# Performance work log

Hardware: AMD Instinct MI355X
Metric: run time of the kernel (lower is better)

## Reference

```python
import jax, jax.numpy as jnp
import numpy as np

B, S, H, E, V, P = 64, 1024, 512, 512, 32000, 40


def setup_inputs() -> dict:
    key = jax.random.key(0)
    ks = jax.random.split(key, 18)
    s = 0.05  # weight scale to keep tanh/sigmoid in active range
    inp = {}
    inp["input_token"] = jax.random.randint(ks[0], (B,), 0, V, dtype=jnp.int32)
    inp["hidden"] = jax.random.normal(ks[1], (1, B, H), jnp.float32)
    inp["cell"] = jax.random.normal(ks[2], (1, B, H), jnp.float32)
    inp["encoder_outputs"] = jax.random.normal(ks[3], (B, S, H), jnp.float32)
    pos_ids = jax.random.randint(ks[4], (B, S), 0, P)
    inp["pos_onehot"] = jax.nn.one_hot(pos_ids, P, dtype=jnp.float32)
    inp["src_mask"] = jnp.zeros((B, S), dtype=bool)  # no PAD (avoids all -inf rows)
    # learned parameters (torch Linear convention: y = x @ W.T + b)
    inp["embed_table"] = jax.random.normal(ks[5], (V, E), jnp.float32) * s
    inp["W_s"] = jax.random.normal(ks[6], (H, H), jnp.float32) * s
    inp["W_h"] = jax.random.normal(ks[7], (H, H), jnp.float32) * s
    inp["V_w"] = jax.random.normal(ks[8], (H,), jnp.float32) * s
    inp["W_p"] = jax.random.normal(ks[9], (P,), jnp.float32) * s
    inp["b_p"] = jax.random.normal(ks[10], (), jnp.float32) * s
    inp["W_ih"] = jax.random.normal(ks[11], (4 * H, E + H), jnp.float32) * s
    inp["W_hh"] = jax.random.normal(ks[12], (4 * H, H), jnp.float32) * s
    inp["b_ih"] = jax.random.normal(ks[13], (4 * H,), jnp.float32) * s
    inp["b_hh"] = jax.random.normal(ks[14], (4 * H,), jnp.float32) * s
    inp["W_out"] = jax.random.normal(ks[15], (V, H), jnp.float32) * s
    inp["b_out"] = jax.random.normal(ks[16], (V,), jnp.float32) * s
    return inp


def reference(input_token, hidden, cell, encoder_outputs, pos_onehot, src_mask,
              embed_table, W_s, W_h, V_w, W_p, b_p,
              W_ih, W_hh, b_ih, b_hh, W_out, b_out):
    # embedding (dropout is identity in eval)
    emb = embed_table[input_token]                                  # (B, E)
    q = hidden[-1]                                                  # (B, H)
    # POS-gated Bahdanau attention
    qs = q @ W_s.T                                                  # (B, H)
    eh = jnp.einsum('bsh,kh->bsk', encoder_outputs, W_h)            # (B, S, H)
    energy = jnp.tanh(qs[:, None, :] + eh)                          # (B, S, H)
    scores = jnp.einsum('bsh,h->bs', energy, V_w)                   # (B, S)
    gate = jax.nn.sigmoid(pos_onehot @ W_p + b_p)                   # (B, S)
    gated = jnp.where(src_mask, jnp.float32(-1e30), scores * gate)
    attn = jax.nn.softmax(gated, axis=-1)                           # (B, S)
    context = jnp.einsum('bs,bsh->bh', attn, encoder_outputs)       # (B, H)
    # single-step, single-layer LSTM (torch gate order: i, f, g, o)
    lstm_in = jnp.concatenate([emb, context], axis=-1)              # (B, E+H)
    gates = lstm_in @ W_ih.T + hidden[0] @ W_hh.T + b_ih + b_hh     # (B, 4H)
    i, f, g, o = jnp.split(gates, 4, axis=-1)
    c1 = jax.nn.sigmoid(f) * cell[0] + jax.nn.sigmoid(i) * jnp.tanh(g)
    h1 = jax.nn.sigmoid(o) * jnp.tanh(c1)                           # (B, H)
    pred = h1 @ W_out.T + b_out                                     # (B, V)
    return (pred, h1[None], c1[None], attn)
```

## Files before the change

kernel.cpp:

```cpp
#include <hip/hip_runtime.h>

#define BB 64
#define SS 1024
#define HH 512
#define EE 512
#define VV 32000
#define PP 40

typedef __attribute__((ext_vector_type(8))) __bf16 bf16x8;
typedef __attribute__((ext_vector_type(4))) float f32x4;
typedef __attribute__((ext_vector_type(8))) unsigned short us8_t;
typedef __attribute__((ext_vector_type(4))) unsigned short us4_t;

__device__ inline float fast_tanh(float x) {
    float e = __expf(-2.0f * fabsf(x));
    float t = (1.0f - e) / (1.0f + e);
    return copysignf(t, x);
}
__device__ inline float sigmf(float x) { return 1.0f / (1.0f + __expf(-x)); }

__device__ inline unsigned int cvtpk(float lo, float hi) {
    unsigned int r;
    asm("v_cvt_pk_bf16_f32 %0, %1, %2" : "=v"(r) : "v"(lo), "v"(hi));
    return r;
}
__device__ inline us8_t pack8c(float4 x, float4 y) {
    union { unsigned int u[4]; us8_t v; } r;
    r.u[0] = cvtpk(x.x, x.y); r.u[1] = cvtpk(x.z, x.w);
    r.u[2] = cvtpk(y.x, y.y); r.u[3] = cvtpk(y.z, y.w);
    return r.v;
}
__device__ inline us8_t pack8v(f32x4 a, f32x4 b) {
    union { unsigned int u[4]; us8_t v; } r;
    r.u[0] = cvtpk(a[0], a[1]); r.u[1] = cvtpk(a[2], a[3]);
    r.u[2] = cvtpk(b[0], b[1]); r.u[3] = cvtpk(b[2], b[3]);
    return r.v;
}

typedef __attribute__((address_space(1))) const unsigned char gas_t;
typedef __attribute__((address_space(3))) unsigned char las_t;
__device__ inline void gload16(const void* g, void* l) {
    __builtin_amdgcn_global_load_lds((gas_t*)g, (las_t*)l, 16, 0, 0);
}

__global__ __launch_bounds__(256)
void k_pre(const float* __restrict__ hidden, const float* __restrict__ Ws,
           const float* __restrict__ Wh, const float* __restrict__ pos,
           const float* __restrict__ Wp, const float* __restrict__ bp,
           unsigned short* __restrict__ wh16, float* __restrict__ qs,
           float* __restrict__ gate, float* __restrict__ ctx) {
    int blk = blockIdx.x, t = threadIdx.x;
    if (blk < 64) {
        __shared__ float hb[HH];
        int b = blk;
        for (int i = t; i < HH; i += 256) hb[i] = hidden[b * HH + i];
        __syncthreads();
        for (int n = t; n < HH; n += 256) {
            const float* wr = Ws + (size_t)n * HH;
            float acc = 0.0f;
#pragma unroll 4
            for (int k = 0; k < HH; k += 4) {
                float4 w = *(const float4*)(wr + k);
                acc += w.x * hb[k] + w.y * hb[k + 1] + w.z * hb[k + 2] + w.w * hb[k + 3];
            }
            qs[b * HH + n] = acc;
        }
    } else if (blk < 96) {
        int base = (blk - 64) * 8192 + t * 4;
#pragma unroll
        for (int j = 0; j < 8; ++j) {
            int idx = base + j * 1024;
            float4 x = *(const float4*)(Wh + idx);
            union { unsigned int u[2]; us4_t v; } r;
            r.u[0] = cvtpk(x.x, x.y); r.u[1] = cvtpk(x.z, x.w);
            *(us4_t*)(wh16 + idx) = r.v;
        }
    } else if (blk < 352) {
        int idx = (blk - 96) * 256 + t;
        const float* pr = pos + (size_t)idx * PP;
        float acc = bp[0];
#pragma unroll
        for (int j = 0; j < 10; ++j) {
            float4 x = *(const float4*)(pr + j * 4);
            acc += x.x * Wp[j * 4] + x.y * Wp[j * 4 + 1] + x.z * Wp[j * 4 + 2] + x.w * Wp[j * 4 + 3];
        }
        gate[idx] = sigmf(acc);
    } else {
        int idx = (blk - 352) * 256 + t;
#pragma unroll
        for (int j = 0; j < 16; ++j) ctx[idx * 16 + j] = 0.0f;
    }
}

__global__ __launch_bounds__(512)
void k_scores(const float* __restrict__ enc,
              const unsigned short* __restrict__ wh16,
              const float* __restrict__ qs, const float* __restrict__ Vw,
              float* __restrict__ part) {
    __shared__ float As[2][4096];
    __shared__ unsigned short Bs[2][8192];
    __shared__ float pbuf[4][128];
    int bid = blockIdx.x;
    int nh = bid >> 9, rest = bid & 511;
    int b = rest >> 3, sc = rest & 7;
    int s0 = sc * 128, n0 = nh * 256;
    int tid = threadIdx.x;
    int w = tid >> 6, lane = tid & 63;
    int wm = w >> 2, wn = w & 3;
    int l15 = lane & 15, lq = lane >> 4;

    float qv[4], vw[4];
#pragma unroll
    for (int nf = 0; nf < 4; ++nf) {
        int n = n0 + wn * 64 + nf * 16 + l15;
        qv[nf] = qs[b * HH + n];
        vw[nf] = Vw[n];
    }

    unsigned int colbA = (unsigned int)(((lane & 7) * 16) ^ ((lane >> 3) << 4));
    unsigned int colbB = (unsigned int)(((lane & 3) * 16) ^ (((lane >> 3) & 3) << 4));
    const char* gA0 = (const char*)(enc + (size_t)(b * SS + s0) * HH);
    const char* gB0 = (const char*)(wh16 + (size_t)n0 * HH);
    int aRowS = w * 8 + (lane >> 3);
    int bRowS = w * 16 + (lane >> 2);
    int ldsOff = w * 1024 + lane * 16;

    int aRowB[4], akey[4], bRowB[4], bkey[4];
#pragma unroll
    for (int mf = 0; mf < 4; ++mf) {
        int r = wm * 64 + mf * 16 + l15;
        aRowB[mf] = r * 128;
        akey[mf] = (r & 7) << 4;
    }
#pragma unroll
    for (int nf = 0; nf < 4; ++nf) {
        int r = wn * 64 + nf * 16 + l15;
        bRowB[nf] = r * 64;
        bkey[nf] = ((r >> 1) & 3) << 4;
    }

    f32x4 acc[4][4];
#pragma unroll
    for (int mf = 0; mf < 4; ++mf)
#pragma unroll
        for (int nf = 0; nf < 4; ++nf) acc[mf][nf] = (f32x4){0.f, 0.f, 0.f, 0.f};

#define STAGE(BUF, KT)                                                          \
    {                                                                           \
        _Pragma("unroll")                                                       \
        for (int p = 0; p < 2; ++p) {                                           \
            const char* ga = gA0 + (size_t)(p * 64 + aRowS) * 2048 +            \
                             (KT) * 128 + colbA;                                \
            gload16(ga, (char*)As[BUF] + p * 8192 + ldsOff);                    \
            const char* gb = gB0 + (size_t)(p * 128 + bRowS) * 1024 +           \
                             (KT) * 64 + colbB;                                 \
            gload16(gb, (char*)Bs[BUF] + p * 8192 + ldsOff);                    \
        }                                                                       \
    }

#define COMPUTE(BUF)                                                            \
    {                                                                           \
        us8_t af[4], bf[4];                                                     \
        _Pragma("unroll")                                                       \
        for (int mf = 0; mf < 4; ++mf) {                                        \
            const char* pa = (const char*)As[BUF] + aRowB[mf];                  \
            f32x4 a0 = *(const f32x4*)(pa + ((lq * 32) ^ akey[mf]));            \
            f32x4 a1 = *(const f32x4*)(pa + ((lq * 32 + 16) ^ akey[mf]));       \
            af[mf] = pack8v(a0, a1);                                            \
        }                                                                       \
        _Pragma("unroll")                                                       \
        for (int nf = 0; nf < 4; ++nf)                                          \
            bf[nf] = *(const us8_t*)((const char*)Bs[BUF] + bRowB[nf] +         \
                                     ((lq * 16) ^ bkey[nf]));                   \
        _Pragma("unroll")                                                       \
        for (int mf = 0; mf < 4; ++mf)                                          \
            _Pragma("unroll")                                                   \
            for (int nf = 0; nf < 4; ++nf)                                      \
                acc[mf][nf] = __builtin_amdgcn_mfma_f32_16x16x32_bf16(          \
                    __builtin_bit_cast(bf16x8, af[mf]),                         \
                    __builtin_bit_cast(bf16x8, bf[nf]), acc[mf][nf], 0, 0, 0);  \
    }

    STAGE(0, 0);
#pragma unroll
    for (int kt = 0; kt < 16; ++kt) {
        if (kt < 15) {
            STAGE((kt + 1) & 1, kt + 1);
            asm volatile("s_waitcnt vmcnt(4)" ::: "memory");
        } else {
            asm volatile("s_waitcnt vmcnt(0)" ::: "memory");
        }
        __builtin_amdgcn_s_barrier();
        COMPUTE(kt & 1);
        __builtin_amdgcn_s_barrier();
    }
#undef STAGE
#undef COMPUTE

#pragma unroll
    for (int mf = 0; mf < 4; ++mf)
#pragma unroll
        for (int r = 0; r < 4; ++r) {
            float p = 0.0f;
#pragma unroll
            for (int nf = 0; nf < 4; ++nf)
                p += vw[nf] * fast_tanh(acc[mf][nf][r] + qv[nf]);
            p += __shfl_xor(p, 1, 64);
            p += __shfl_xor(p, 2, 64);
            p += __shfl_xor(p, 4, 64);
            p += __shfl_xor(p, 8, 64);
            if (l15 == 0) pbuf[wn][wm * 64 + mf * 16 + lq * 4 + r] = p;
        }
    __syncthreads();
    if (tid < 128) {
        part[nh * (BB * SS) + b * SS + s0 + tid] =
            pbuf[0][tid] + pbuf[1][tid] + pbuf[2][tid] + pbuf[3][tid];
    }
}

__global__ __launch_bounds__(256)
void k_context(const float* __restrict__ enc, const float* __restrict__ part,
               const float* __restrict__ gate, const unsigned char* __restrict__ mask,
               float* __restrict__ attn, float* __restrict__ ctx) {
    int b = blockIdx.x >> 4, chunk = blockIdx.x & 15;
    int s0 = chunk * 64, t = threadIdx.x;
    int w = t >> 6, ln = t & 63;
    float sum = 0.0f;
#pragma unroll
    for (int j = 0; j < 4; ++j) {
        int s = j * 256 + t;
        float raw = part[b * SS + s] + part[BB * SS + b * SS + s];
        float v = mask[b * SS + s] ? -1e30f : raw * gate[b * SS + s];
        sum += __expf(v);
    }
#pragma unroll
    for (int off = 1; off < 64; off <<= 1) sum += __shfl_xor(sum, off, 64);
    __shared__ float sl[4];
    if (ln == 0) sl[w] = sum;
    __syncthreads();
    float inv = 1.0f / (sl[0] + sl[1] + sl[2] + sl[3]);

    __shared__ float aw[64];
    if (t < 64) {
        int s = s0 + t;
        float raw = part[b * SS + s] + part[BB * SS + b * SS + s];
        float v = mask[b * SS + s] ? -1e30f : raw * gate[b * SS + s];
        float a = __expf(v) * inv;
        aw[t] = a;
        attn[b * SS + s] = a;
    }
    __syncthreads();

    const float* eb = enc + ((size_t)(b * SS + s0)) * HH + 2 * t;
    float a0 = 0.f, a1 = 0.f;
#pragma unroll 4
    for (int s = 0; s < 64; ++s) {
        float2 u = *(const float2*)(eb + (size_t)s * HH);
        a0 += aw[s] * u.x;
        a1 += aw[s] * u.y;
    }
    atomicAdd(&ctx[b * HH + 2 * t], a0);
    atomicAdd(&ctx[b * HH + 2 * t + 1], a1);
}

__global__ __launch_bounds__(256)
void k_build(const int* __restrict__ tok, const float* __restrict__ embt,
             const float* __restrict__ ctx, const float* __restrict__ hidden,
             unsigned short* __restrict__ li16, unsigned short* __restrict__ h16v) {
    int b = blockIdx.x, t = threadIdx.x;
    const float* er = embt + (size_t)tok[b] * EE;
    for (int i = 2 * t; i < HH; i += 512) {
        *(unsigned int*)(li16 + b * 1024 + i) = cvtpk(er[i], er[i + 1]);
        *(unsigned int*)(li16 + b * 1024 + 512 + i) = cvtpk(ctx[b * HH + i], ctx[b * HH + i + 1]);
        *(unsigned int*)(h16v + b * HH + i) = cvtpk(hidden[b * HH + i], hidden[b * HH + i + 1]);
    }
}

__global__ __launch_bounds__(256)
void k_gates(const unsigned short* __restrict__ li16, const unsigned short* __restrict__ h16v,
             const float* __restrict__ Wih, const float* __restrict__ Whh,
             float* __restrict__ gpart) {
    int nt = blockIdx.x >> 2, ksl = blockIdx.x & 3;
    int wave = threadIdx.x >> 6, lane = threadIdx.x & 63;
    int l15 = lane & 15, lq = lane >> 4, k0 = lq * 8;
    int n0w = nt * 128 + wave * 32;
    f32x4 acc[4][2];
#pragma unroll
    for (int mf = 0; mf < 4; ++mf)
#pragma unroll
        for (int nf = 0; nf < 2; ++nf) acc[mf][nf] = (f32x4){0.f, 0.f, 0.f, 0.f};

    for (int ks = 0; ks < 12; ++ks) {
        int kg = ksl * 384 + ks * 32;
        us8_t af[4];
        if (kg < 1024) {
#pragma unroll
            for (int mf = 0; mf < 4; ++mf)
                af[mf] = *(const us8_t*)(li16 + (mf * 16 + l15) * 1024 + kg + k0);
        } else {
#pragma unroll
            for (int mf = 0; mf < 4; ++mf)
                af[mf] = *(const us8_t*)(h16v + (mf * 16 + l15) * 512 + (kg - 1024) + k0);
        }
#pragma unroll
        for (int nf = 0; nf < 2; ++nf) {
            int n = n0w + nf * 16 + l15;
            us8_t bu;
            if (kg < 1024) {
                const float* wr = Wih + (size_t)n * 1024 + kg + k0;
                bu = pack8c(*(const float4*)wr, *(const float4*)(wr + 4));
            } else {
                const float* wr = Whh + (size_t)n * 512 + (kg - 1024) + k0;
                bu = pack8c(*(const float4*)wr, *(const float4*)(wr + 4));
            }
#pragma unroll
            for (int mf = 0; mf < 4; ++mf)
                acc[mf][nf] = __builtin_amdgcn_mfma_f32_16x16x32_bf16(
                    __builtin_bit_cast(bf16x8, af[mf]),
                    __builtin_bit_cast(bf16x8, bu), acc[mf][nf], 0, 0, 0);
        }
    }
#pragma unroll
    for (int mf = 0; mf < 4; ++mf)
#pragma unroll
        for (int nf = 0; nf < 2; ++nf)
#pragma unroll
            for (int r = 0; r < 4; ++r) {
                int row = mf * 16 + lq * 4 + r;
                int n = n0w + nf * 16 + l15;
                gpart[ksl * (BB * 2048) + row * 2048 + n] = acc[mf][nf][r];
            }
}

__global__ __launch_bounds__(512)
void k_lstm(const float* __restrict__ gpart, const float* __restrict__ bih,
            const float* __restrict__ bhh, const float* __restrict__ cell,
            float* __restrict__ oh, float* __restrict__ oc,
            unsigned short* __restrict__ h116) {
    int b = blockIdx.x, t = threadIdx.x;
    float gi = bih[t] + bhh[t];
    float gf = bih[512 + t] + bhh[512 + t];
    float gg = bih[1024 + t] + bhh[1024 + t];
    float go = bih[1536 + t] + bhh[1536 + t];
#pragma unroll
    for (int ksl = 0; ksl < 4; ++ksl) {
        const float* gp = gpart + ksl * (BB * 2048) + b * 2048;
        gi += gp[t];
        gf += gp[512 + t];
        gg += gp[1024 + t];
        go += gp[1536 + t];
    }
    float c0 = cell[b * HH + t];
    float c1 = sigmf(gf) * c0 + sigmf(gi) * fast_tanh(gg);
    float h1 = sigmf(go) * fast_tanh(c1);
    oh[b * HH + t] = h1;
    oc[b * HH + t] = c1;
    h116[b * HH + t] = (unsigned short)(cvtpk(h1, h1) & 0xffffu);
}

__global__ __launch_bounds__(512)
void k_pred(const unsigned short* __restrict__ h116, const float* __restrict__ Wout,
            const float* __restrict__ bout, float* __restrict__ pred) {
    int wave = threadIdx.x >> 6, lane = threadIdx.x & 63;
    int l15 = lane & 15, lq = lane >> 4, k0 = lq * 8;
    int n = blockIdx.x * 128 + wave * 16 + l15;
    f32x4 acc[4];
#pragma unroll
    for (int mf = 0; mf < 4; ++mf) acc[mf] = (f32x4){0.f, 0.f, 0.f, 0.f};
    const float* wr = Wout + (size_t)n * HH;
#pragma unroll 4
    for (int ks = 0; ks < 16; ++ks) {
        float4 x = *(const float4*)(wr + ks * 32 + k0);
        float4 y = *(const float4*)(wr + ks * 32 + k0 + 4);
        us8_t bu = pack8c(x, y);
#pragma unroll
        for (int mf = 0; mf < 4; ++mf) {
            us8_t au = *(const us8_t*)(h116 + (mf * 16 + l15) * 512 + ks * 32 + k0);
            acc[mf] = __builtin_amdgcn_mfma_f32_16x16x32_bf16(
                __builtin_bit_cast(bf16x8, au),
                __builtin_bit_cast(bf16x8, bu), acc[mf], 0, 0, 0);
        }
    }
    float bo = bout[n];
#pragma unroll
    for (int mf = 0; mf < 4; ++mf)
#pragma unroll
        for (int r = 0; r < 4; ++r) {
            int row = mf * 16 + lq * 4 + r;
            pred[(size_t)row * VV + n] = acc[mf][r] + bo;
        }
}

extern "C" void kernel_launch(void* const* d_in, const int* in_sizes, int n_in,
                              void* d_out, int out_size, void* d_ws, size_t ws_size,
                              hipStream_t stream) {
    const int* tok = (const int*)d_in[0];
    const float* hidden = (const float*)d_in[1];
    const float* cell = (const float*)d_in[2];
    const float* enc = (const float*)d_in[3];
    const float* pos = (const float*)d_in[4];
    const unsigned char* mask = (const unsigned char*)d_in[5];
    const float* embt = (const float*)d_in[6];
    const float* Ws = (const float*)d_in[7];
    const float* Wh = (const float*)d_in[8];
    const float* Vw = (const float*)d_in[9];
    const float* Wp = (const float*)d_in[10];
    const float* bp = (const float*)d_in[11];
    const float* Wih = (const float*)d_in[12];
    const float* Whh = (const float*)d_in[13];
    const float* bih = (const float*)d_in[14];
    const float* bhh = (const float*)d_in[15];
    const float* Wout = (const float*)d_in[16];
    const float* bout = (const float*)d_in[17];

    float* out = (float*)d_out;
    float* pred = out;
    float* out_h = out + 2048000;
    float* out_c = out + 2080768;
    float* attn = out + 2113536;

    char* wsb = (char*)d_ws;
    unsigned short* wh16 = (unsigned short*)(wsb);
    float* qs = (float*)(wsb + (512 << 10));
    float* gate = (float*)(wsb + (640 << 10));
    float* part = (float*)(wsb + (896 << 10));
    float* ctx = (float*)(wsb + (1408 << 10));
    unsigned short* li16 = (unsigned short*)(wsb + (1536 << 10));
    unsigned short* h16v = (unsigned short*)(wsb + (1664 << 10));
    float* gpart = (float*)(wsb + (1728 << 10));
    unsigned short* h116 = (unsigned short*)(wsb + (3776 << 10));

    hipLaunchKernelGGL(k_pre, dim3(360), dim3(256), 0, stream,
                       hidden, Ws, Wh, pos, Wp, bp, wh16, qs, gate, ctx);
    hipLaunchKernelGGL(k_scores, dim3(1024), dim3(512), 0, stream,
                       enc, wh16, qs, Vw, part);
    hipLaunchKernelGGL(k_context, dim3(1024), dim3(256), 0, stream,
                       enc, part, gate, mask, attn, ctx);
    hipLaunchKernelGGL(k_build, dim3(64), dim3(256), 0, stream,
                       tok, embt, ctx, hidden, li16, h16v);
    hipLaunchKernelGGL(k_gates, dim3(64), dim3(256), 0, stream, li16, h16v, Wih, Whh, gpart);
    hipLaunchKernelGGL(k_lstm, dim3(64), dim3(512), 0, stream,
                       gpart, bih, bhh, cell, out_h, out_c, h116);
    hipLaunchKernelGGL(k_pred, dim3(250), dim3(512), 0, stream, h116, Wout, bout, pred);
}
```

Measured before the change: 171.4 us.

## Convert encoder tile to bf16 in registers before LDS and drop k_build kernel

In the scores GEMM, the encoder A tile is now loaded from global into registers, converted to bf16 once, and written to LDS. The old path staged fp32 data with async global-to-LDS loads and converted it to bf16 on every fragment read. This halves the A-tile LDS footprint and read traffic, and the loop now uses a single barrier per k-step instead of two. Separately, the k_build kernel is removed: embedding and hidden bf16 packing move into k_pre, and k_gates converts the fp32 context on the fly. This saves one launch, at the cost of a register-mediated A load that may expose more global latency.

Result: slower. 183.1 us (+6.8%).

```diff
diff --git a/kernel.cpp b/kernel.cpp
--- a/kernel.cpp
+++ b/kernel.cpp
@@ -30,12 +30,6 @@
     r.u[2] = cvtpk(y.x, y.y); r.u[3] = cvtpk(y.z, y.w);
     return r.v;
 }
-__device__ inline us8_t pack8v(f32x4 a, f32x4 b) {
-    union { unsigned int u[4]; us8_t v; } r;
-    r.u[0] = cvtpk(a[0], a[1]); r.u[1] = cvtpk(a[2], a[3]);
-    r.u[2] = cvtpk(b[0], b[1]); r.u[3] = cvtpk(b[2], b[3]);
-    return r.v;
-}
 
 typedef __attribute__((address_space(1))) const unsigned char gas_t;
 typedef __attribute__((address_space(3))) unsigned char las_t;
@@ -47,8 +41,10 @@
 void k_pre(const float* __restrict__ hidden, const float* __restrict__ Ws,
            const float* __restrict__ Wh, const float* __restrict__ pos,
            const float* __restrict__ Wp, const float* __restrict__ bp,
+           const int* __restrict__ tok, const float* __restrict__ embt,
            unsigned short* __restrict__ wh16, float* __restrict__ qs,
-           float* __restrict__ gate, float* __restrict__ ctx) {
+           float* __restrict__ gate, float* __restrict__ ctx,
+           unsigned short* __restrict__ emb16, unsigned short* __restrict__ h16v) {
     int blk = blockIdx.x, t = threadIdx.x;
     if (blk < 64) {
         __shared__ float hb[HH];
@@ -65,6 +61,11 @@
             }
             qs[b * HH + n] = acc;
         }
+        const float* er = embt + (size_t)tok[b] * EE;
+        for (int i = 2 * t; i < HH; i += 512) {
+            *(unsigned int*)(emb16 + b * 512 + i) = cvtpk(er[i], er[i + 1]);
+            *(unsigned int*)(h16v + b * 512 + i) = cvtpk(hb[i], hb[i + 1]);
+        }
     } else if (blk < 96) {
         int base = (blk - 64) * 8192 + t * 4;
 #pragma unroll
@@ -97,8 +98,8 @@
               const unsigned short* __restrict__ wh16,
               const float* __restrict__ qs, const float* __restrict__ Vw,
               float* __restrict__ part) {
-    __shared__ float As[2][4096];
-    __shared__ unsigned short Bs[2][8192];
+    __shared__ unsigned short Abuf[2][4096];
+    __shared__ unsigned short Bbuf[2][8192];
     __shared__ float pbuf[4][128];
     int bid = blockIdx.x;
     int nh = bid >> 9, rest = bid & 511;
@@ -117,25 +118,27 @@
         vw[nf] = Vw[n];
     }
 
-    unsigned int colbA = (unsigned int)(((lane & 7) * 16) ^ ((lane >> 3) << 4));
-    unsigned int colbB = (unsigned int)(((lane & 3) * 16) ^ (((lane >> 3) & 3) << 4));
-    const char* gA0 = (const char*)(enc + (size_t)(b * SS + s0) * HH);
+    int arow = tid >> 2, aseg = tid & 3;
+    int akeyw = (arow >> 1) & 3;
+    const float* aSrc = enc + (size_t)(b * SS + s0 + arow) * HH + aseg * 8;
+    int aWr = arow * 64 + ((aseg ^ akeyw) << 4);
+
+    unsigned int colbB = (unsigned int)((((lane & 3) ^ ((lane >> 3) & 3)) & 3) << 4);
     const char* gB0 = (const char*)(wh16 + (size_t)n0 * HH);
-    int aRowS = w * 8 + (lane >> 3);
     int bRowS = w * 16 + (lane >> 2);
-    int ldsOff = w * 1024 + lane * 16;
-
-    int aRowB[4], akey[4], bRowB[4], bkey[4];
+    int ldsOffB = w * 1024 + lane * 16;
+
+    int aRdB[4], akey[4], bRdB[4], bkey[4];
 #pragma unroll
     for (int mf = 0; mf < 4; ++mf) {
         int r = wm * 64 + mf * 16 + l15;
-        aRowB[mf] = r * 128;
-        akey[mf] = (r & 7) << 4;
+        aRdB[mf] = r * 64;
+        akey[mf] = ((r >> 1) & 3) << 4;
     }
 #pragma unroll
     for (int nf = 0; nf < 4; ++nf) {
         int r = wn * 64 + nf * 16 + l15;
-        bRowB[nf] = r * 64;
+        bRdB[nf] = r * 64;
         bkey[nf] = ((r >> 1) & 3) << 4;
     }
 
@@ -144,57 +147,67 @@
     for (int mf = 0; mf < 4; ++mf)
 #pragma unroll
         for (int nf = 0; nf < 4; ++nf) acc[mf][nf] = (f32x4){0.f, 0.f, 0.f, 0.f};
-
-#define STAGE(BUF, KT)                                                          \
-    {                                                                           \
-        _Pragma("unroll")                                                       \
-        for (int p = 0; p < 2; ++p) {                                           \
-            const char* ga = gA0 + (size_t)(p * 64 + aRowS) * 2048 +            \
-                             (KT) * 128 + colbA;                                \
-            gload16(ga, (char*)As[BUF] + p * 8192 + ldsOff);                    \
-            const char* gb = gB0 + (size_t)(p * 128 + bRowS) * 1024 +           \
-                             (KT) * 64 + colbB;                                 \
-            gload16(gb, (char*)Bs[BUF] + p * 8192 + ldsOff);                    \
-        }                                                                       \
-    }
 
 #define COMPUTE(BUF)                                                            \
     {                                                                           \
-        us8_t af[4], bf[4];                                                     \
+        us8_t af[4], bfr[4];                                                    \
         _Pragma("unroll")                                                       \
-        for (int mf = 0; mf < 4; ++mf) {                                        \
-            const char* pa = (const char*)As[BUF] + aRowB[mf];                  \
-            f32x4 a0 = *(const f32x4*)(pa + ((lq * 32) ^ akey[mf]));            \
-            f32x4 a1 = *(const f32x4*)(pa + ((lq * 32 + 16) ^ akey[mf]));       \
-            af[mf] = pack8v(a0, a1);                                            \
-        }                                                                       \
+        for (int mf = 0; mf < 4; ++mf)                                          \
+            af[mf] = *(const us8_t*)((const char*)Abuf[BUF] + aRdB[mf] +        \
+                                     ((lq << 4) ^ akey[mf]));                   \
         _Pragma("unroll")                                                       \
         for (int nf = 0; nf < 4; ++nf)                                          \
-            bf[nf] = *(const us8_t*)((const char*)Bs[BUF] + bRowB[nf] +         \
-                                     ((lq * 16) ^ bkey[nf]));                   \
+            bfr[nf] = *(const us8_t*)((const char*)Bbuf[BUF] + bRdB[nf] +       \
+                                      ((lq << 4) ^ bkey[nf]));                  \
         _Pragma("unroll")                                                       \
         for (int mf = 0; mf < 4; ++mf)                                          \
             _Pragma("unroll")                                                   \
             for (int nf = 0; nf < 4; ++nf)                                      \
                 acc[mf][nf] = __builtin_amdgcn_mfma_f32_16x16x32_bf16(          \
                     __builtin_bit_cast(bf16x8, af[mf]),                         \
-                    __builtin_bit_cast(bf16x8, bf[nf]), acc[mf][nf], 0, 0, 0);  \
-    }
-
-    STAGE(0, 0);
+                    __builtin_bit_cast(bf16x8, bfr[nf]), acc[mf][nf], 0, 0, 0); \
+    }
+
+    float4 xa0 = *(const float4*)(aSrc);
+    float4 xa1 = *(const float4*)(aSrc + 4);
+#pragma unroll
+    for (int p = 0; p < 2; ++p)
+        gload16(gB0 + (size_t)(p * 128 + bRowS) * 1024 + colbB,
+                (char*)Bbuf[0] + p * 8192 + ldsOffB);
+    asm volatile("s_waitcnt vmcnt(2)" ::: "memory");
+    *(us8_t*)((char*)Abuf[0] + aWr) = pack8c(xa0, xa1);
+    xa0 = *(const float4*)(aSrc + 32);
+    xa1 = *(const float4*)(aSrc + 36);
+    asm volatile("s_waitcnt vmcnt(2)" ::: "memory");
+    asm volatile("s_waitcnt lgkmcnt(0)" ::: "memory");
+    __builtin_amdgcn_s_barrier();
+
 #pragma unroll
     for (int kt = 0; kt < 16; ++kt) {
         if (kt < 15) {
-            STAGE((kt + 1) & 1, kt + 1);
-            asm volatile("s_waitcnt vmcnt(4)" ::: "memory");
-        } else {
+#pragma unroll
+            for (int p = 0; p < 2; ++p)
+                gload16(gB0 + (size_t)(p * 128 + bRowS) * 1024 + (kt + 1) * 64 + colbB,
+                        (char*)Bbuf[(kt + 1) & 1] + p * 8192 + ldsOffB);
+            asm volatile("s_waitcnt vmcnt(2)" ::: "memory");
+            *(us8_t*)((char*)Abuf[(kt + 1) & 1] + aWr) = pack8c(xa0, xa1);
+            if (kt < 14) {
+                const float* g = aSrc + (kt + 2) * 32;
+                xa0 = *(const float4*)(g);
+                xa1 = *(const float4*)(g + 4);
+            }
+        }
+        COMPUTE(kt & 1);
+        if (kt < 14) {
+            asm volatile("s_waitcnt vmcnt(2)" ::: "memory");
+        } else if (kt == 14) {
             asm volatile("s_waitcnt vmcnt(0)" ::: "memory");
         }
-        __builtin_amdgcn_s_barrier();
-        COMPUTE(kt & 1);
-        __builtin_amdgcn_s_barrier();
-    }
-#undef STAGE
+        if (kt < 15) {
+            asm volatile("s_waitcnt lgkmcnt(0)" ::: "memory");
+            __builtin_amdgcn_s_barrier();
+        }
+    }
 #undef COMPUTE
 
 #pragma unroll
@@ -264,20 +277,8 @@
 }
 
 __global__ __launch_bounds__(256)
-void k_build(const int* __restrict__ tok, const float* __restrict__ embt,
-             const float* __restrict__ ctx, const float* __restrict__ hidden,
-             unsigned short* __restrict__ li16, unsigned short* __restrict__ h16v) {
-    int b = blockIdx.x, t = threadIdx.x;
-    const float* er = embt + (size_t)tok[b] * EE;
-    for (int i = 2 * t; i < HH; i += 512) {
-        *(unsigned int*)(li16 + b * 1024 + i) = cvtpk(er[i], er[i + 1]);
-        *(unsigned int*)(li16 + b * 1024 + 512 + i) = cvtpk(ctx[b * HH + i], ctx[b * HH + i + 1]);
-        *(unsigned int*)(h16v + b * HH + i) = cvtpk(hidden[b * HH + i], hidden[b * HH + i + 1]);
-    }
-}
-
-__global__ __launch_bounds__(256)
-void k_gates(const unsigned short* __restrict__ li16, const unsigned short* __restrict__ h16v,
+void k_gates(const unsigned short* __restrict__ emb16, const float* __restrict__ ctx,
+             const unsigned short* __restrict__ h16v,
              const float* __restrict__ Wih, const float* __restrict__ Whh,
              float* __restrict__ gpart) {
     int nt = blockIdx.x >> 2, ksl = blockIdx.x & 3;
@@ -293,10 +294,16 @@
     for (int ks = 0; ks < 12; ++ks) {
         int kg = ksl * 384 + ks * 32;
         us8_t af[4];
-        if (kg < 1024) {
+        if (kg < 512) {
 #pragma unroll
             for (int mf = 0; mf < 4; ++mf)
-                af[mf] = *(const us8_t*)(li16 + (mf * 16 + l15) * 1024 + kg + k0);
+                af[mf] = *(const us8_t*)(emb16 + (mf * 16 + l15) * 512 + kg + k0);
+        } else if (kg < 1024) {
+#pragma unroll
+            for (int mf = 0; mf < 4; ++mf) {
+                const float* cr = ctx + (size_t)(mf * 16 + l15) * 512 + (kg - 512) + k0;
+                af[mf] = pack8c(*(const float4*)cr, *(const float4*)(cr + 4));
+            }
         } else {
 #pragma unroll
             for (int mf = 0; mf < 4; ++mf)
@@ -425,20 +432,20 @@
     float* gate = (float*)(wsb + (640 << 10));
     float* part = (float*)(wsb + (896 << 10));
     float* ctx = (float*)(wsb + (1408 << 10));
-    unsigned short* li16 = (unsigned short*)(wsb + (1536 << 10));
-    unsigned short* h16v = (unsigned short*)(wsb + (1664 << 10));
-    float* gpart = (float*)(wsb + (1728 << 10));
-    unsigned short* h116 = (unsigned short*)(wsb + (3776 << 10));
+    unsigned short* emb16 = (unsigned short*)(wsb + (1536 << 10));
+    unsigned short* h16v = (unsigned short*)(wsb + (1600 << 10));
+    float* gpart = (float*)(wsb + (1664 << 10));
+    unsigned short* h116 = (unsigned short*)(wsb + (3712 << 10));
 
     hipLaunchKernelGGL(k_pre, dim3(360), dim3(256), 0, stream,
-                       hidden, Ws, Wh, pos, Wp, bp, wh16, qs, gate, ctx);
+                       hidden, Ws, Wh, pos, Wp, bp, tok, embt,
+                       wh16, qs, gate, ctx, emb16, h16v);
     hipLaunchKernelGGL(k_scores, dim3(1024), dim3(512), 0, stream,
                        enc, wh16, qs, Vw, part);
     hipLaunchKernelGGL(k_context, dim3(1024), dim3(256), 0, stream,
                        enc, part, gate, mask, attn, ctx);
-    hipLaunchKernelGGL(k_build, dim3(64), dim3(256), 0, stream,
-                       tok, embt, ctx, hidden, li16, h16v);
-    hipLaunchKernelGGL(k_gates, dim3(64), dim3(256), 0, stream, li16, h16v, Wih, Whh, gpart);
+    hipLaunchKernelGGL(k_gates, dim3(64), dim3(256), 0, stream,
+                       emb16, ctx, h16v, Wih, Whh, gpart);
     hipLaunchKernelGGL(k_lstm, dim3(64), dim3(512), 0, stream,
                        gpart, bih, bhh, cell, out_h, out_c, h116);
     hipLaunchKernelGGL(k_pred, dim3(250), dim3(512), 0, stream, h116, Wout, bout, pred);
```

## Fuse attention context accumulation into scores kernel with unnormalized softmax

Applied to the files above, without the earlier changes.

Each scores block now covers the full hidden width with 1024 threads, so the encoder tile is staged once instead of once per N-half. The block then computes exp(gated score) in the epilogue and accumulates an unnormalized context and softmax denominator with atomics. A small finalize kernel divides by the denominator, which removes the separate k_context pass that re-read the encoder and partial scores. This adds more atomics on ctx and denominators and a larger LDS footprint per block. It relies on the scores being small enough to exponentiate without subtracting a max, as the old code already did.

Result: slower. 178.5 us (+4.1%).

```diff
diff --git a/kernel.cpp b/kernel.cpp
--- a/kernel.cpp
+++ b/kernel.cpp
@@ -48,7 +48,8 @@
            const float* __restrict__ Wh, const float* __restrict__ pos,
            const float* __restrict__ Wp, const float* __restrict__ bp,
            unsigned short* __restrict__ wh16, float* __restrict__ qs,
-           float* __restrict__ gate, float* __restrict__ ctx) {
+           float* __restrict__ gate, float* __restrict__ ctxu,
+           float* __restrict__ denom) {
     int blk = blockIdx.x, t = threadIdx.x;
     if (blk < 64) {
         __shared__ float hb[HH];
@@ -88,31 +89,33 @@
     } else {
         int idx = (blk - 352) * 256 + t;
 #pragma unroll
-        for (int j = 0; j < 16; ++j) ctx[idx * 16 + j] = 0.0f;
-    }
-}
-
-__global__ __launch_bounds__(512)
+        for (int j = 0; j < 16; ++j) ctxu[idx * 16 + j] = 0.0f;
+        if (blk == 352 && t < 64) denom[t] = 0.0f;
+    }
+}
+
+__global__ __launch_bounds__(1024)
 void k_scores(const float* __restrict__ enc,
               const unsigned short* __restrict__ wh16,
               const float* __restrict__ qs, const float* __restrict__ Vw,
-              float* __restrict__ part) {
+              const float* __restrict__ gate, const unsigned char* __restrict__ mask,
+              float* __restrict__ part, float* __restrict__ ctxu,
+              float* __restrict__ denom) {
     __shared__ float As[2][4096];
-    __shared__ unsigned short Bs[2][8192];
+    __shared__ unsigned short Bs[2][16384];
     __shared__ float pbuf[4][128];
-    int bid = blockIdx.x;
-    int nh = bid >> 9, rest = bid & 511;
-    int b = rest >> 3, sc = rest & 7;
-    int s0 = sc * 128, n0 = nh * 256;
+    __shared__ float ebuf[128];
+    int b = blockIdx.x >> 3, sc = blockIdx.x & 7;
+    int s0 = sc * 128;
     int tid = threadIdx.x;
     int w = tid >> 6, lane = tid & 63;
     int wm = w >> 2, wn = w & 3;
     int l15 = lane & 15, lq = lane >> 4;
 
-    float qv[4], vw[4];
-#pragma unroll
-    for (int nf = 0; nf < 4; ++nf) {
-        int n = n0 + wn * 64 + nf * 16 + l15;
+    float qv[8], vw[8];
+#pragma unroll
+    for (int nf = 0; nf < 8; ++nf) {
+        int n = wn * 128 + nf * 16 + l15;
         qv[nf] = qs[b * HH + n];
         vw[nf] = Vw[n];
     }
@@ -120,62 +123,61 @@
     unsigned int colbA = (unsigned int)(((lane & 7) * 16) ^ ((lane >> 3) << 4));
     unsigned int colbB = (unsigned int)(((lane & 3) * 16) ^ (((lane >> 3) & 3) << 4));
     const char* gA0 = (const char*)(enc + (size_t)(b * SS + s0) * HH);
-    const char* gB0 = (const char*)(wh16 + (size_t)n0 * HH);
+    const char* gB0 = (const char*)wh16;
     int aRowS = w * 8 + (lane >> 3);
     int bRowS = w * 16 + (lane >> 2);
     int ldsOff = w * 1024 + lane * 16;
 
-    int aRowB[4], akey[4], bRowB[4], bkey[4];
-#pragma unroll
-    for (int mf = 0; mf < 4; ++mf) {
-        int r = wm * 64 + mf * 16 + l15;
+    int aRowB[2], akey[2], bRowB[8], bkey[8];
+#pragma unroll
+    for (int mf = 0; mf < 2; ++mf) {
+        int r = wm * 32 + mf * 16 + l15;
         aRowB[mf] = r * 128;
         akey[mf] = (r & 7) << 4;
     }
 #pragma unroll
-    for (int nf = 0; nf < 4; ++nf) {
-        int r = wn * 64 + nf * 16 + l15;
+    for (int nf = 0; nf < 8; ++nf) {
+        int r = wn * 128 + nf * 16 + l15;
         bRowB[nf] = r * 64;
         bkey[nf] = ((r >> 1) & 3) << 4;
     }
 
-    f32x4 acc[4][4];
-#pragma unroll
-    for (int mf = 0; mf < 4; ++mf)
-#pragma unroll
-        for (int nf = 0; nf < 4; ++nf) acc[mf][nf] = (f32x4){0.f, 0.f, 0.f, 0.f};
+    f32x4 acc[2][8];
+#pragma unroll
+    for (int mf = 0; mf < 2; ++mf)
+#pragma unroll
+        for (int nf = 0; nf < 8; ++nf) acc[mf][nf] = (f32x4){0.f, 0.f, 0.f, 0.f};
 
 #define STAGE(BUF, KT)                                                          \
     {                                                                           \
+        const char* ga = gA0 + (size_t)aRowS * 2048 + (KT) * 128 + colbA;       \
+        gload16(ga, (char*)As[BUF] + ldsOff);                                   \
         _Pragma("unroll")                                                       \
         for (int p = 0; p < 2; ++p) {                                           \
-            const char* ga = gA0 + (size_t)(p * 64 + aRowS) * 2048 +            \
-                             (KT) * 128 + colbA;                                \
-            gload16(ga, (char*)As[BUF] + p * 8192 + ldsOff);                    \
-            const char* gb = gB0 + (size_t)(p * 128 + bRowS) * 1024 +           \
+            const char* gb = gB0 + (size_t)(p * 256 + bRowS) * 1024 +           \
                              (KT) * 64 + colbB;                                 \
-            gload16(gb, (char*)Bs[BUF] + p * 8192 + ldsOff);                    \
+            gload16(gb, (char*)Bs[BUF] + p * 16384 + ldsOff);                   \
         }                                                                       \
     }
 
 #define COMPUTE(BUF)                                                            \
     {                                                                           \
-        us8_t af[4], bf[4];                                                     \
+        us8_t af[2], bf[8];                                                     \
         _Pragma("unroll")                                                       \
-        for (int mf = 0; mf < 4; ++mf) {                                        \
+        for (int mf = 0; mf < 2; ++mf) {                                        \
             const char* pa = (const char*)As[BUF] + aRowB[mf];                  \
             f32x4 a0 = *(const f32x4*)(pa + ((lq * 32) ^ akey[mf]));            \
             f32x4 a1 = *(const f32x4*)(pa + ((lq * 32 + 16) ^ akey[mf]));       \
             af[mf] = pack8v(a0, a1);                                            \
         }                                                                       \
         _Pragma("unroll")                                                       \
-        for (int nf = 0; nf < 4; ++nf)                                          \
+        for (int nf = 0; nf < 8; ++nf)                                          \
             bf[nf] = *(const us8_t*)((const char*)Bs[BUF] + bRowB[nf] +         \
                                      ((lq * 16) ^ bkey[nf]));                   \
         _Pragma("unroll")                                                       \
-        for (int mf = 0; mf < 4; ++mf)                                          \
+        for (int mf = 0; mf < 2; ++mf)                                          \
             _Pragma("unroll")                                                   \
-            for (int nf = 0; nf < 4; ++nf)                                      \
+            for (int nf = 0; nf < 8; ++nf)                                      \
                 acc[mf][nf] = __builtin_amdgcn_mfma_f32_16x16x32_bf16(          \
                     __builtin_bit_cast(bf16x8, af[mf]),                         \
                     __builtin_bit_cast(bf16x8, bf[nf]), acc[mf][nf], 0, 0, 0);  \
@@ -186,7 +188,7 @@
     for (int kt = 0; kt < 16; ++kt) {
         if (kt < 15) {
             STAGE((kt + 1) & 1, kt + 1);
-            asm volatile("s_waitcnt vmcnt(4)" ::: "memory");
+            asm volatile("s_waitcnt vmcnt(3)" ::: "memory");
         } else {
             asm volatile("s_waitcnt vmcnt(0)" ::: "memory");
         }
@@ -198,69 +200,56 @@
 #undef COMPUTE
 
 #pragma unroll
-    for (int mf = 0; mf < 4; ++mf)
+    for (int mf = 0; mf < 2; ++mf)
 #pragma unroll
         for (int r = 0; r < 4; ++r) {
             float p = 0.0f;
 #pragma unroll
-            for (int nf = 0; nf < 4; ++nf)
+            for (int nf = 0; nf < 8; ++nf)
                 p += vw[nf] * fast_tanh(acc[mf][nf][r] + qv[nf]);
             p += __shfl_xor(p, 1, 64);
             p += __shfl_xor(p, 2, 64);
             p += __shfl_xor(p, 4, 64);
             p += __shfl_xor(p, 8, 64);
-            if (l15 == 0) pbuf[wn][wm * 64 + mf * 16 + lq * 4 + r] = p;
+            if (l15 == 0) pbuf[wn][wm * 32 + mf * 16 + lq * 4 + r] = p;
         }
     __syncthreads();
+
     if (tid < 128) {
-        part[nh * (BB * SS) + b * SS + s0 + tid] =
-            pbuf[0][tid] + pbuf[1][tid] + pbuf[2][tid] + pbuf[3][tid];
+        int s = s0 + tid;
+        float p = pbuf[0][tid] + pbuf[1][tid] + pbuf[2][tid] + pbuf[3][tid];
+        float v = mask[b * SS + s] ? -1e30f : p * gate[b * SS + s];
+        float e = __expf(v);
+        ebuf[tid] = e;
+        part[b * SS + s] = e;
+    }
+    __syncthreads();
+    if (tid < 64) {
+        float de = ebuf[tid] + ebuf[tid + 64];
+#pragma unroll
+        for (int off = 1; off < 64; off <<= 1) de += __shfl_xor(de, off, 64);
+        if (tid == 0) atomicAdd(&denom[b], de);
+    }
+
+    {
+        int h = tid & 511, sh = tid >> 9;
+        const float* ep = enc + (size_t)(b * SS + s0 + sh * 64) * HH + h;
+        const float* eb = &ebuf[sh * 64];
+        float sum = 0.0f;
+#pragma unroll 4
+        for (int j = 0; j < 64; ++j) sum += eb[j] * ep[(size_t)j * HH];
+        atomicAdd(&ctxu[b * HH + h], sum);
     }
 }
 
 __global__ __launch_bounds__(256)
-void k_context(const float* __restrict__ enc, const float* __restrict__ part,
-               const float* __restrict__ gate, const unsigned char* __restrict__ mask,
-               float* __restrict__ attn, float* __restrict__ ctx) {
-    int b = blockIdx.x >> 4, chunk = blockIdx.x & 15;
-    int s0 = chunk * 64, t = threadIdx.x;
-    int w = t >> 6, ln = t & 63;
-    float sum = 0.0f;
-#pragma unroll
-    for (int j = 0; j < 4; ++j) {
-        int s = j * 256 + t;
-        float raw = part[b * SS + s] + part[BB * SS + b * SS + s];
-        float v = mask[b * SS + s] ? -1e30f : raw * gate[b * SS + s];
-        sum += __expf(v);
-    }
-#pragma unroll
-    for (int off = 1; off < 64; off <<= 1) sum += __shfl_xor(sum, off, 64);
-    __shared__ float sl[4];
-    if (ln == 0) sl[w] = sum;
-    __syncthreads();
-    float inv = 1.0f / (sl[0] + sl[1] + sl[2] + sl[3]);
-
-    __shared__ float aw[64];
-    if (t < 64) {
-        int s = s0 + t;
-        float raw = part[b * SS + s] + part[BB * SS + b * SS + s];
-        float v = mask[b * SS + s] ? -1e30f : raw * gate[b * SS + s];
-        float a = __expf(v) * inv;
-        aw[t] = a;
-        attn[b * SS + s] = a;
-    }
-    __syncthreads();
-
-    const float* eb = enc + ((size_t)(b * SS + s0)) * HH + 2 * t;
-    float a0 = 0.f, a1 = 0.f;
-#pragma unroll 4
-    for (int s = 0; s < 64; ++s) {
-        float2 u = *(const float2*)(eb + (size_t)s * HH);
-        a0 += aw[s] * u.x;
-        a1 += aw[s] * u.y;
-    }
-    atomicAdd(&ctx[b * HH + 2 * t], a0);
-    atomicAdd(&ctx[b * HH + 2 * t + 1], a1);
+void k_fin(const float* __restrict__ part, const float* __restrict__ ctxu,
+           const float* __restrict__ denom, float* __restrict__ attn,
+           float* __restrict__ ctx) {
+    int b = blockIdx.x, t = threadIdx.x;
+    float inv = 1.0f / denom[b];
+    for (int s = t; s < SS; s += 256) attn[b * SS + s] = part[b * SS + s] * inv;
+    for (int h = t; h < HH; h += 256) ctx[b * HH + h] = ctxu[b * HH + h] * inv;
 }
 
 __global__ __launch_bounds__(256)
@@ -424,18 +413,20 @@
     float* qs = (float*)(wsb + (512 << 10));
     float* gate = (float*)(wsb + (640 << 10));
     float* part = (float*)(wsb + (896 << 10));
-    float* ctx = (float*)(wsb + (1408 << 10));
-    unsigned short* li16 = (unsigned short*)(wsb + (1536 << 10));
-    unsigned short* h16v = (unsigned short*)(wsb + (1664 << 10));
-    float* gpart = (float*)(wsb + (1728 << 10));
-    unsigned short* h116 = (unsigned short*)(wsb + (3776 << 10));
+    float* ctxu = (float*)(wsb + (1152 << 10));
+    float* ctx = (float*)(wsb + (1280 << 10));
+    float* denom = (float*)(wsb + (1408 << 10));
+    unsigned short* li16 = (unsigned short*)(wsb + (1412 << 10));
+    unsigned short* h16v = (unsigned short*)(wsb + (1540 << 10));
+    float* gpart = (float*)(wsb + (1604 << 10));
+    unsigned short* h116 = (unsigned short*)(wsb + (3652 << 10));
 
     hipLaunchKernelGGL(k_pre, dim3(360), dim3(256), 0, stream,
-                       hidden, Ws, Wh, pos, Wp, bp, wh16, qs, gate, ctx);
-    hipLaunchKernelGGL(k_scores, dim3(1024), dim3(512), 0, stream,
-                       enc, wh16, qs, Vw, part);
-    hipLaunchKernelGGL(k_context, dim3(1024), dim3(256), 0, stream,
-                       enc, part, gate, mask, attn, ctx);
+                       hidden, Ws, Wh, pos, Wp, bp, wh16, qs, gate, ctxu, denom);
+    hipLaunchKernelGGL(k_scores, dim3(512), dim3(1024), 0, stream,
+                       enc, wh16, qs, Vw, gate, mask, part, ctxu, denom);
+    hipLaunchKernelGGL(k_fin, dim3(64), dim3(256), 0, stream,
+                       part, ctxu, denom, attn, ctx);
     hipLaunchKernelGGL(k_build, dim3(64), dim3(256), 0, stream,
                        tok, embt, ctx, hidden, li16, h16v);
     hipLaunchKernelGGL(k_gates, dim3(64), dim3(256), 0, stream, li16, h16v, Wih, Whh, gpart);
```
